# Kernel optimization log

Hardware: AMD Instinct MI355X
Metric: run time of the kernel (lower is better)

Reference implementation:

```python
import jax, jax.numpy as jnp
import numpy as np

B, S, D = 2, 2048, 1024
E, K = 8, 2
H = 1792  # round_up(int(1024*5/3)=1706, 256)


def setup_inputs() -> dict:
    key = jax.random.key(0)
    k1, k2, k3, k4, k5 = jax.random.split(key, 5)
    scale = 0.02
    x = jax.random.normal(k1, (B, S, D), dtype=jnp.float32)
    gate_w = jax.random.normal(k2, (E, D), dtype=jnp.float32) * scale   # nn.Linear(D,E).weight
    w_gate = jax.random.normal(k3, (E, D, H), dtype=jnp.float32) * scale
    w_up = jax.random.normal(k4, (E, D, H), dtype=jnp.float32) * scale
    w_down = jax.random.normal(k5, (E, H, D), dtype=jnp.float32) * scale
    return {"x": x, "gate_w": gate_w, "w_gate": w_gate, "w_up": w_up, "w_down": w_down}


def reference(x, gate_w, w_gate, w_up, w_down):
    b, s, d = x.shape
    x_flat = x.reshape(-1, d)                      # [T, D]
    # Gate computed in bf16 (torch autocast) then cast back to f32.
    logits = (x_flat.astype(jnp.bfloat16) @ gate_w.T.astype(jnp.bfloat16)).astype(jnp.float32)  # [T, E]
    topk_w, topk_idx = jax.lax.top_k(logits, K)    # [T, K]
    topk_w = jax.nn.softmax(topk_w, axis=-1)
    probs = jax.nn.softmax(logits, axis=-1)        # [T, E]
    mean_probs = probs.mean(0)                     # [E]
    load_balance_loss = E * jnp.sum(mean_probs ** 2)
    # Per-token combine weight for each expert (equivalent to sort/split/index_add combine).
    combine = jnp.sum(jax.nn.one_hot(topk_idx, E, dtype=x_flat.dtype) * topk_w[..., None], axis=1)  # [T, E]
    out = jnp.zeros_like(x_flat)
    for e in range(E):  # fixed small expert loop; math identical to grouped dispatch
        g = x_flat @ w_gate[e]                     # [T, H]
        u = x_flat @ w_up[e]                       # [T, H]
        y = (jax.nn.silu(g) * u) @ w_down[e]       # [T, D]
        out = out + y * combine[:, e:e + 1]
    return out.reshape(b, s, d), load_balance_loss, mean_probs
```

## Files before the change

kernel.cpp:

```cpp
#include <hip/hip_runtime.h>
#include <stdint.h>

#define TT 4096
#define DD 1024
#define EE 8
#define HH 1792
#define MP 10240
#define MT128 80

typedef __attribute__((ext_vector_type(8))) short short8;
typedef __attribute__((ext_vector_type(4))) short short4v;
typedef __attribute__((ext_vector_type(4))) float f32x4;

static __device__ __forceinline__ unsigned short f2bf(float f) {
  union { float f; uint32_t u; } v; v.f = f;
  return (unsigned short)((v.u + 0x7fffu + ((v.u >> 16) & 1u)) >> 16);
}
static __device__ __forceinline__ float bf2f(unsigned short h) {
  union { uint32_t u; float f; } v; v.u = ((uint32_t)h) << 16;
  return v.f;
}

static __device__ __forceinline__ void gll16(const void* g, const void* l) {
  __builtin_amdgcn_global_load_lds(
      (const __attribute__((address_space(1))) unsigned int*)g,
      (__attribute__((address_space(3))) unsigned int*)l, 16, 0, 0);
}

__global__ __launch_bounds__(256) void prep_weights(
    const float* __restrict__ w_gate, const float* __restrict__ w_up,
    const float* __restrict__ w_down, unsigned short* __restrict__ wguT,
    unsigned short* __restrict__ wdT) {
  __shared__ float L0[64][65];
  __shared__ float L1[64][65];
  const int tid = threadIdx.x;
  const int lr = tid >> 2, lc = (tid & 3) * 16;
  int bid = blockIdx.x;
  if (bid < 3584) {
    const int e = bid / 448, r = bid % 448;
    const int bx = r / 28, by = r % 28;
    const size_t so = (size_t)e * DD * HH + (size_t)(bx * 64) * HH + by * 64;
    const float* g = w_gate + so;
    const float* u = w_up + so;
#pragma unroll
    for (int q = 0; q < 4; ++q) {
      const f32x4 vg = *(const f32x4*)(g + (size_t)lr * HH + lc + 4 * q);
      const f32x4 vu = *(const f32x4*)(u + (size_t)lr * HH + lc + 4 * q);
#pragma unroll
      for (int j = 0; j < 4; ++j) {
        L0[lr][lc + 4 * q + j] = vg[j];
        L1[lr][lc + 4 * q + j] = vu[j];
      }
    }
    __syncthreads();
    unsigned short b0[16], b1[16];
#pragma unroll
    for (int q = 0; q < 16; ++q) {
      b0[q] = f2bf(L0[lc + q][lr]);
      b1[q] = f2bf(L1[lc + q][lr]);
    }
    const int h = by * 64 + lr;
    const int pg = (h >> 4) * 32 + (h & 15);
    unsigned short* dst = wguT + (size_t)e * 2 * HH * DD + (size_t)bx * 64 + lc;
    *(short8*)(dst + (size_t)pg * DD) = *(const short8*)&b0[0];
    *(short8*)(dst + (size_t)pg * DD + 8) = *(const short8*)&b0[8];
    *(short8*)(dst + (size_t)(pg + 16) * DD) = *(const short8*)&b1[0];
    *(short8*)(dst + (size_t)(pg + 16) * DD + 8) = *(const short8*)&b1[8];
  } else {
    bid -= 3584;
    const int e = bid / 448, r = bid % 448;
    const int bx = r / 16, by = r % 16;
    const float* src = w_down + (size_t)e * HH * DD + (size_t)(bx * 64) * DD + by * 64;
#pragma unroll
    for (int q = 0; q < 4; ++q) {
      const f32x4 v = *(const f32x4*)(src + (size_t)lr * DD + lc + 4 * q);
#pragma unroll
      for (int j = 0; j < 4; ++j) L0[lr][lc + 4 * q + j] = v[j];
    }
    __syncthreads();
    unsigned short b0[16];
#pragma unroll
    for (int q = 0; q < 16; ++q) b0[q] = f2bf(L0[lc + q][lr]);
    const int d = by * 64 + lr;
    unsigned short* dst = wdT + (size_t)e * DD * HH + (size_t)d * HH + bx * 64 + lc;
    *(short8*)(dst) = *(const short8*)&b0[0];
    *(short8*)(dst + 8) = *(const short8*)&b0[8];
  }
}

__global__ __launch_bounds__(256) void gate_kernel(
    const float* __restrict__ x, const float* __restrict__ gw,
    float* __restrict__ combine, float* __restrict__ probs, int2* __restrict__ topk) {
  const int lane = threadIdx.x & 63;
  const int wave = threadIdx.x >> 6;
  const int t = blockIdx.x * 4 + wave;
  const float* xr = x + (size_t)t * DD;
  float acc[EE];
#pragma unroll
  for (int e = 0; e < EE; ++e) acc[e] = 0.f;
#pragma unroll
  for (int i = 0; i < DD / 256; ++i) {
    const int d = (i * 64 + lane) * 4;
    const f32x4 xv = *(const f32x4*)(xr + d);
    float xb[4];
#pragma unroll
    for (int j = 0; j < 4; ++j) xb[j] = bf2f(f2bf(xv[j]));
#pragma unroll
    for (int e = 0; e < EE; ++e) {
      const f32x4 gv = *(const f32x4*)(gw + e * DD + d);
#pragma unroll
      for (int j = 0; j < 4; ++j) acc[e] += xb[j] * bf2f(f2bf(gv[j]));
    }
  }
#pragma unroll
  for (int e = 0; e < EE; ++e) {
#pragma unroll
    for (int off = 32; off > 0; off >>= 1)
      acc[e] += __shfl_xor(acc[e], off, 64);
  }
  if (lane == 0) {
    float lg[EE];
#pragma unroll
    for (int e = 0; e < EE; ++e) lg[e] = bf2f(f2bf(acc[e]));
    float m1 = -1e30f, m2 = -1e30f; int i1 = 0, i2 = 0;
#pragma unroll
    for (int e = 0; e < EE; ++e) {
      const float v = lg[e];
      if (v > m1) { m2 = m1; i2 = i1; m1 = v; i1 = e; }
      else if (v > m2) { m2 = v; i2 = e; }
    }
    const float e2 = expf(m2 - m1);
    const float w1 = 1.f / (1.f + e2);
    const float w2 = e2 * w1;
    float cb[EE];
#pragma unroll
    for (int e = 0; e < EE; ++e) cb[e] = 0.f;
    cb[i1] = w1; cb[i2] += w2;
    float p[EE]; float s = 0.f;
#pragma unroll
    for (int e = 0; e < EE; ++e) { p[e] = expf(lg[e] - m1); s += p[e]; }
    const float inv = 1.f / s;
#pragma unroll
    for (int e = 0; e < EE; ++e) {
      combine[(size_t)t * EE + e] = cb[e];
      probs[(size_t)t * EE + e] = p[e] * inv;
    }
    topk[t] = make_int2(i1, i2);
  }
}

__global__ __launch_bounds__(512) void route_kernel(
    const int2* __restrict__ topk, const float* __restrict__ combine,
    const float* __restrict__ probs, int* __restrict__ tok_list,
    float* __restrict__ wt_list, int* __restrict__ tab128, float* __restrict__ tail) {
  const int lane = threadIdx.x & 63;
  const int e = threadIdx.x >> 6;
  __shared__ int cnts[EE], offs[EE];
  __shared__ float sm[EE];
  int cnt = 0;
  for (int i = 0; i < TT / 64; ++i) {
    const int2 k2 = topk[i * 64 + lane];
    cnt += __popcll(__ballot(k2.x == e || k2.y == e));
  }
  if (lane == 0) cnts[e] = cnt;
  __syncthreads();
  if (threadIdx.x == 0) {
    int off = 0, n128 = 0;
    for (int f = 0; f < EE; ++f) {
      offs[f] = off;
      const int pc = (cnts[f] + 127) & ~127;
      for (int j = 0; j < (pc >> 7); ++j) {
        tab128[2 * n128] = f; tab128[2 * n128 + 1] = off + 128 * j; ++n128;
      }
      off += pc;
    }
    for (; n128 < MT128; ++n128) { tab128[2 * n128] = -1; tab128[2 * n128 + 1] = 0; }
  }
  __syncthreads();
  int pos = offs[e];
  for (int i = 0; i < TT / 64; ++i) {
    const int t = i * 64 + lane;
    const int2 k2 = topk[t];
    const bool sel = (k2.x == e || k2.y == e);
    const unsigned long long m = __ballot(sel);
    if (sel) {
      const int p = pos + __popcll(m & ((1ull << lane) - 1ull));
      tok_list[p] = t;
      wt_list[p] = combine[(size_t)t * EE + e];
    }
    pos += __popcll(m);
  }
  const int pc = (cnt + 127) & ~127;
  for (int s = cnt + lane; s < pc; s += 64) {
    tok_list[offs[e] + s] = 0;
    wt_list[offs[e] + s] = 0.f;
  }
  float racc = 0.f;
  for (int t = lane; t < TT; t += 64) racc += probs[(size_t)t * EE + e];
#pragma unroll
  for (int off = 32; off > 0; off >>= 1) racc += __shfl_xor(racc, off, 64);
  if (lane == 0) {
    const float m = racc * (1.f / TT);
    sm[e] = m;
    tail[1 + e] = m;
  }
  __syncthreads();
  if (threadIdx.x == 0) {
    float loss = 0.f;
#pragma unroll
    for (int f = 0; f < EE; ++f) loss += sm[f] * sm[f];
    tail[0] = (float)EE * loss;
  }
}

__global__ __launch_bounds__(256) void gather_x(
    const float* __restrict__ x, const int* __restrict__ tok_list,
    const int* __restrict__ tab128, unsigned short* __restrict__ xg) {
  const int e = tab128[2 * blockIdx.x];
  if (e < 0) return;
  const int row0 = tab128[2 * blockIdx.x + 1] + blockIdx.y * 16;
  const int tid = threadIdx.x;
#pragma unroll
  for (int i = 0; i < 16; ++i) {
    const int row = row0 + i;
    const int tok = tok_list[row];
    const f32x4 v = *(const f32x4*)(x + (size_t)tok * DD + tid * 4);
    unsigned short b[4] = {f2bf(v[0]), f2bf(v[1]), f2bf(v[2]), f2bf(v[3])};
    *(short4v*)(xg + (size_t)row * DD + tid * 4) = *(const short4v*)b;
  }
}

template <int MODE>
__global__ __launch_bounds__(256, 3) void gemm128(
    const unsigned short* __restrict__ Ab, const unsigned short* __restrict__ Bb,
    const int* __restrict__ tab, const int* __restrict__ tok_list,
    const float* __restrict__ wt_list, unsigned short* __restrict__ act,
    float* __restrict__ out) {
  constexpr int K   = (MODE == 0) ? DD : HH;
  constexpr int NBR = (MODE == 0) ? 2 * HH : DD;
  constexpr int NNT = NBR / 128;
  __shared__ unsigned short As[128 * 64];
  __shared__ unsigned short Bs[128 * 64];

  const int nwg = gridDim.x;
  const int wgid = (blockIdx.x & 7) * (nwg >> 3) + (blockIdx.x >> 3);
  const int mt = wgid / NNT, nt = wgid % NNT;
  const int e = tab[2 * mt];
  if (e < 0) return;
  const int row0 = tab[2 * mt + 1];
  const int n0 = nt * 128;

  const int tid = threadIdx.x, lane = tid & 63, wave = tid >> 6;
  const int wm = (wave >> 1) * 64, wn = (wave & 1) * 64;
  const int fr = lane & 15, hi = lane >> 4;

  const unsigned short* At = Ab + (size_t)row0 * K;
  const unsigned short* Bt = Bb + ((size_t)e * NBR + n0) * K;

  const int srel = tid * 16;
  const int srow0 = srel >> 7;
  const int sch = (srel >> 4) & 7;

  f32x4 acc[4][4];
#pragma unroll
  for (int i = 0; i < 4; ++i)
#pragma unroll
    for (int j = 0; j < 4; ++j) acc[i][j] = (f32x4){0.f, 0.f, 0.f, 0.f};

  for (int k0 = 0; k0 < K; k0 += 64) {
#pragma unroll
    for (int q = 0; q < 4; ++q) {
      const int row = q * 32 + srow0;
      gll16(At + (size_t)row * K + k0 + ((sch ^ (row & 7)) << 3),
            (const char*)As + q * 4096 + srel);
    }
#pragma unroll
    for (int q = 0; q < 4; ++q) {
      const int row = q * 32 + srow0;
      gll16(Bt + (size_t)row * K + k0 + ((sch ^ (row & 7)) << 3),
            (const char*)Bs + q * 4096 + srel);
    }
    __syncthreads();
#pragma unroll
    for (int kc = 0; kc < 2; ++kc) {
      short8 a[4], b[4];
#pragma unroll
      for (int i = 0; i < 4; ++i) {
        const int row = wm + i * 16 + fr;
        a[i] = *(const short8*)((const char*)As + ((row * 128 + kc * 64 + hi * 16) ^ ((row & 7) << 4)));
      }
#pragma unroll
      for (int j = 0; j < 4; ++j) {
        const int row = wn + j * 16 + fr;
        b[j] = *(const short8*)((const char*)Bs + ((row * 128 + kc * 64 + hi * 16) ^ ((row & 7) << 4)));
      }
#pragma unroll
      for (int i = 0; i < 4; ++i)
#pragma unroll
        for (int j = 0; j < 4; ++j)
          acc[i][j] = __builtin_amdgcn_mfma_f32_16x16x32_bf16(a[i], b[j], acc[i][j], 0, 0, 0);
    }
    __syncthreads();
  }

  const int r4 = hi * 4;
  if constexpr (MODE == 0) {
#pragma unroll
    for (int i = 0; i < 4; ++i)
#pragma unroll
      for (int r = 0; r < 4; ++r) {
        const int row = row0 + wm + i * 16 + r4 + r;
#pragma unroll
        for (int jj = 0; jj < 2; ++jj) {
          const float g = acc[i][2 * jj][r], u = acc[i][2 * jj + 1][r];
          const int nb = n0 + wn + jj * 32;
          const int h = ((nb >> 5) << 4) + fr;
          act[(size_t)row * HH + h] = f2bf((g / (1.f + expf(-g))) * u);
        }
      }
  } else {
#pragma unroll
    for (int i = 0; i < 4; ++i)
#pragma unroll
      for (int r = 0; r < 4; ++r) {
        const int rl = row0 + wm + i * 16 + r4 + r;
        const int tok = tok_list[rl];
        const float wt = wt_list[rl];
        if (wt != 0.f) {
#pragma unroll
          for (int j = 0; j < 4; ++j)
            unsafeAtomicAdd(&out[(size_t)tok * DD + n0 + wn + j * 16 + fr],
                            acc[i][j][r] * wt);
        }
      }
  }
}

extern "C" void kernel_launch(void* const* d_in, const int* in_sizes, int n_in,
                              void* d_out, int out_size, void* d_ws, size_t ws_size,
                              hipStream_t stream) {
  const float* x      = (const float*)d_in[0];
  const float* gw     = (const float*)d_in[1];
  const float* w_gate = (const float*)d_in[2];
  const float* w_up   = (const float*)d_in[3];
  const float* w_down = (const float*)d_in[4];
  float* out = (float*)d_out;
  float* tail = out + (size_t)TT * DD;

  char* w = (char*)d_ws;
  size_t o = 0;
  auto carve = [&](size_t bytes) { char* p = w + o; o += (bytes + 255) & ~255ull; return p; };
  unsigned short* wguT = (unsigned short*)carve((size_t)EE * 2 * HH * DD * 2);
  unsigned short* wdT  = (unsigned short*)carve((size_t)EE * DD * HH * 2);
  unsigned short* xg   = (unsigned short*)carve((size_t)MP * DD * 2);
  unsigned short* act  = (unsigned short*)carve((size_t)MP * HH * 2);
  float* combine = (float*)carve((size_t)TT * EE * 4);
  float* probs   = (float*)carve((size_t)TT * EE * 4);
  int2* topk     = (int2*)carve((size_t)TT * 8);
  int* tok_list  = (int*)carve((size_t)MP * 4);
  float* wt_list = (float*)carve((size_t)MP * 4);
  int* tab128    = (int*)carve((size_t)MT128 * 8);

  hipMemsetAsync(out, 0, (size_t)TT * DD * sizeof(float), stream);

  prep_weights<<<7168, 256, 0, stream>>>(w_gate, w_up, w_down, wguT, wdT);

  gate_kernel<<<TT / 4, 256, 0, stream>>>(x, gw, combine, probs, topk);
  route_kernel<<<1, 512, 0, stream>>>(topk, combine, probs, tok_list, wt_list, tab128, tail);
  gather_x<<<dim3(MT128, 8), 256, 0, stream>>>(x, tok_list, tab128, xg);

  gemm128<0><<<MT128 * 28, 256, 0, stream>>>(xg, wguT, tab128, nullptr, nullptr, act, nullptr);
  gemm128<1><<<MT128 * 8, 256, 0, stream>>>(act, wdT, tab128, tok_list, wt_list, nullptr, out);
}
```

Before: 277.2 us.

## Fold token gather into up-projection GEMM and emit bf16 x from gate kernel

The gate kernel now writes a bf16 copy of x alongside the logits, and the first grouped GEMM loads its A rows straight from that buffer by indexing through tok_list. This removes the separate gather_x kernel launch and its padded xg staging buffer. The gate kernel also stores just the two top-k weights per token instead of a dense combine table, so route_kernel picks each token's weight from that pair. The cost is an indirect, non-contiguous row access for A in the GEMM and a full-size bf16 write of x in the gate kernel.

```diff
diff --git a/kernel.cpp b/kernel.cpp
--- a/kernel.cpp
+++ b/kernel.cpp
@@ -90,7 +90,8 @@
 
 __global__ __launch_bounds__(256) void gate_kernel(
     const float* __restrict__ x, const float* __restrict__ gw,
-    float* __restrict__ combine, float* __restrict__ probs, int2* __restrict__ topk) {
+    float2* __restrict__ wts, float* __restrict__ probs, int2* __restrict__ topk,
+    unsigned short* __restrict__ xbf) {
   const int lane = threadIdx.x & 63;
   const int wave = threadIdx.x >> 6;
   const int t = blockIdx.x * 4 + wave;
@@ -102,9 +103,11 @@
   for (int i = 0; i < DD / 256; ++i) {
     const int d = (i * 64 + lane) * 4;
     const f32x4 xv = *(const f32x4*)(xr + d);
+    unsigned short us[4];
     float xb[4];
 #pragma unroll
-    for (int j = 0; j < 4; ++j) xb[j] = bf2f(f2bf(xv[j]));
+    for (int j = 0; j < 4; ++j) { us[j] = f2bf(xv[j]); xb[j] = bf2f(us[j]); }
+    *(short4v*)(xbf + (size_t)t * DD + d) = *(const short4v*)us;
 #pragma unroll
     for (int e = 0; e < EE; ++e) {
       const f32x4 gv = *(const f32x4*)(gw + e * DD + d);
@@ -131,26 +134,19 @@
     }
     const float e2 = expf(m2 - m1);
     const float w1 = 1.f / (1.f + e2);
-    const float w2 = e2 * w1;
-    float cb[EE];
-#pragma unroll
-    for (int e = 0; e < EE; ++e) cb[e] = 0.f;
-    cb[i1] = w1; cb[i2] += w2;
     float p[EE]; float s = 0.f;
 #pragma unroll
     for (int e = 0; e < EE; ++e) { p[e] = expf(lg[e] - m1); s += p[e]; }
     const float inv = 1.f / s;
 #pragma unroll
-    for (int e = 0; e < EE; ++e) {
-      combine[(size_t)t * EE + e] = cb[e];
-      probs[(size_t)t * EE + e] = p[e] * inv;
-    }
+    for (int e = 0; e < EE; ++e) probs[(size_t)t * EE + e] = p[e] * inv;
+    wts[t] = make_float2(w1, e2 * w1);
     topk[t] = make_int2(i1, i2);
   }
 }
 
 __global__ __launch_bounds__(512) void route_kernel(
-    const int2* __restrict__ topk, const float* __restrict__ combine,
+    const int2* __restrict__ topk, const float2* __restrict__ wts,
     const float* __restrict__ probs, int* __restrict__ tok_list,
     float* __restrict__ wt_list, int* __restrict__ tab128, float* __restrict__ tail) {
   const int lane = threadIdx.x & 63;
@@ -185,8 +181,9 @@
     const unsigned long long m = __ballot(sel);
     if (sel) {
       const int p = pos + __popcll(m & ((1ull << lane) - 1ull));
+      const float2 w2v = wts[t];
       tok_list[p] = t;
-      wt_list[p] = combine[(size_t)t * EE + e];
+      wt_list[p] = (k2.x == e) ? w2v.x : w2v.y;
     }
     pos += __popcll(m);
   }
@@ -210,23 +207,6 @@
 #pragma unroll
     for (int f = 0; f < EE; ++f) loss += sm[f] * sm[f];
     tail[0] = (float)EE * loss;
-  }
-}
-
-__global__ __launch_bounds__(256) void gather_x(
-    const float* __restrict__ x, const int* __restrict__ tok_list,
-    const int* __restrict__ tab128, unsigned short* __restrict__ xg) {
-  const int e = tab128[2 * blockIdx.x];
-  if (e < 0) return;
-  const int row0 = tab128[2 * blockIdx.x + 1] + blockIdx.y * 16;
-  const int tid = threadIdx.x;
-#pragma unroll
-  for (int i = 0; i < 16; ++i) {
-    const int row = row0 + i;
-    const int tok = tok_list[row];
-    const f32x4 v = *(const f32x4*)(x + (size_t)tok * DD + tid * 4);
-    unsigned short b[4] = {f2bf(v[0]), f2bf(v[1]), f2bf(v[2]), f2bf(v[3])};
-    *(short4v*)(xg + (size_t)row * DD + tid * 4) = *(const short4v*)b;
   }
 }
 
@@ -254,13 +234,23 @@
   const int wm = (wave >> 1) * 64, wn = (wave & 1) * 64;
   const int fr = lane & 15, hi = lane >> 4;
 
-  const unsigned short* At = Ab + (size_t)row0 * K;
   const unsigned short* Bt = Bb + ((size_t)e * NBR + n0) * K;
 
   const int srel = tid * 16;
   const int srow0 = srel >> 7;
   const int sch = (srel >> 4) & 7;
 
+  const unsigned short* srcA[4];
+#pragma unroll
+  for (int q = 0; q < 4; ++q) {
+    const int row = q * 32 + srow0;
+    const int swz = (sch ^ (row & 7)) << 3;
+    if constexpr (MODE == 0)
+      srcA[q] = Ab + (size_t)tok_list[row0 + row] * DD + swz;
+    else
+      srcA[q] = Ab + (size_t)(row0 + row) * K + swz;
+  }
+
   f32x4 acc[4][4];
 #pragma unroll
   for (int i = 0; i < 4; ++i)
@@ -269,11 +259,8 @@
 
   for (int k0 = 0; k0 < K; k0 += 64) {
 #pragma unroll
-    for (int q = 0; q < 4; ++q) {
-      const int row = q * 32 + srow0;
-      gll16(At + (size_t)row * K + k0 + ((sch ^ (row & 7)) << 3),
-            (const char*)As + q * 4096 + srel);
-    }
+    for (int q = 0; q < 4; ++q)
+      gll16(srcA[q] + k0, (const char*)As + q * 4096 + srel);
 #pragma unroll
     for (int q = 0; q < 4; ++q) {
       const int row = q * 32 + srow0;
@@ -352,9 +339,9 @@
   auto carve = [&](size_t bytes) { char* p = w + o; o += (bytes + 255) & ~255ull; return p; };
   unsigned short* wguT = (unsigned short*)carve((size_t)EE * 2 * HH * DD * 2);
   unsigned short* wdT  = (unsigned short*)carve((size_t)EE * DD * HH * 2);
-  unsigned short* xg   = (unsigned short*)carve((size_t)MP * DD * 2);
+  unsigned short* xbf  = (unsigned short*)carve((size_t)TT * DD * 2);
   unsigned short* act  = (unsigned short*)carve((size_t)MP * HH * 2);
-  float* combine = (float*)carve((size_t)TT * EE * 4);
+  float2* wts    = (float2*)carve((size_t)TT * 8);
   float* probs   = (float*)carve((size_t)TT * EE * 4);
   int2* topk     = (int2*)carve((size_t)TT * 8);
   int* tok_list  = (int*)carve((size_t)MP * 4);
@@ -365,10 +352,9 @@
 
   prep_weights<<<7168, 256, 0, stream>>>(w_gate, w_up, w_down, wguT, wdT);
 
-  gate_kernel<<<TT / 4, 256, 0, stream>>>(x, gw, combine, probs, topk);
-  route_kernel<<<1, 512, 0, stream>>>(topk, combine, probs, tok_list, wt_list, tab128, tail);
-  gather_x<<<dim3(MT128, 8), 256, 0, stream>>>(x, tok_list, tab128, xg);
-
-  gemm128<0><<<MT128 * 28, 256, 0, stream>>>(xg, wguT, tab128, nullptr, nullptr, act, nullptr);
+  gate_kernel<<<TT / 4, 256, 0, stream>>>(x, gw, wts, probs, topk, xbf);
+  route_kernel<<<1, 512, 0, stream>>>(topk, wts, probs, tok_list, wt_list, tab128, tail);
+
+  gemm128<0><<<MT128 * 28, 256, 0, stream>>>(xbf, wguT, tab128, tok_list, nullptr, act, nullptr);
   gemm128<1><<<MT128 * 8, 256, 0, stream>>>(act, wdT, tab128, tok_list, wt_list, nullptr, out);
 }
```

Result: no change. 273.4 us (-1.4%).
